# Performance work log

Measured on AMD Instinct MI355X. Metric: run time of the kernel, lower is better.

Reference implementation:

```python
import jax, jax.numpy as jnp
import numpy as np

H = 16  # n_heads


def setup_inputs() -> dict:
    key = jax.random.key(0)
    ks = jax.random.split(key, 11)
    B, S, D = 2, 2048, 1024
    def rn(k, shape, scale=1.0):
        return jax.random.normal(k, shape, dtype=jnp.float32) * scale
    w_scale = 1.0 / np.sqrt(D)
    return {
        "queries": rn(ks[0], (B, S, D)),
        "keys": rn(ks[1], (B, S, D)),
        "values": rn(ks[2], (B, S, D)),
        "Wq": rn(ks[3], (D, D), w_scale), "bq": rn(ks[4], (D,), 0.02),
        "Wk": rn(ks[5], (D, D), w_scale), "bk": rn(ks[6], (D,), 0.02),
        "Wv": rn(ks[7], (D, D), w_scale), "bv": rn(ks[8], (D,), 0.02),
        "Wo": rn(ks[9], (D, D), w_scale), "bo": rn(ks[10], (D,), 0.02),
    }


def _split_heads(x, h):
    # [B, S, D] -> [B, h, S, D/h]
    B, S, D = x.shape
    return x.reshape(B, S, h, D // h).transpose(0, 2, 1, 3)


def reference(queries, keys, values, Wq, bq, Wk, bk, Wv, bv, Wo, bo):
    B, S, D = queries.shape
    Q = _split_heads(queries @ Wq + bq, H)  # [B,h,S,dk]
    K = _split_heads(keys @ Wk + bk, H)
    V = _split_heads(values @ Wv + bv, H)
    # Faithful quirk: scale by sqrt(seq_len), not sqrt(d_k)
    factor = jnp.sqrt(jnp.asarray(S, dtype=Q.dtype))
    scores = jnp.einsum("bhqd,bhkd->bhqk", Q, K) / factor  # [B,h,S,S]
    weights = jax.nn.softmax(scores, axis=-1)
    attn = jnp.einsum("bhqk,bhkd->bhqd", weights, V)  # [B,h,S,dk]
    attn = attn.transpose(0, 2, 1, 3).reshape(B, S, D)  # [B,S,D]
    return attn @ Wo + bo
```

## Files before the change

### kernel.cpp

```cpp
#include <hip/hip_runtime.h>

typedef unsigned short ushort_t;
typedef unsigned int uint_t;
typedef __attribute__((ext_vector_type(8))) short short8;
typedef __attribute__((ext_vector_type(4))) float floatx4;

#define QSCALE 0.03187936f

__device__ __forceinline__ ushort_t f2bf(float f) {
    union { float f; uint_t u; } c; c.f = f;
    uint_t u = c.u;
    return (ushort_t)((u + 0x7fffu + ((u >> 16) & 1u)) >> 16);
}
__device__ __forceinline__ floatx4 mfma16x32(short8 a, short8 b, floatx4 c) {
    return __builtin_amdgcn_mfma_f32_16x16x32_bf16(a, b, c, 0, 0, 0);
}
__device__ __forceinline__ floatx4 zero4() { floatx4 z = {0.f, 0.f, 0.f, 0.f}; return z; }

__device__ __forceinline__ void gload16(const ushort_t* g, ushort_t* l) {
    __builtin_amdgcn_global_load_lds(
        (const __attribute__((address_space(1))) void*)g,
        (__attribute__((address_space(3))) void*)l, 16, 0, 0);
}

__global__ __launch_bounds__(256) void cvt_bf16(
    const float* __restrict__ src, ushort_t* __restrict__ dst)
{
    const int i = (blockIdx.x * 256 + threadIdx.x) * 8;
    float4 f0 = *(const float4*)(src + i);
    float4 f1 = *(const float4*)(src + i + 4);
    __align__(16) ushort_t t[8];
    t[0] = f2bf(f0.x); t[1] = f2bf(f0.y); t[2] = f2bf(f0.z); t[3] = f2bf(f0.w);
    t[4] = f2bf(f1.x); t[5] = f2bf(f1.y); t[6] = f2bf(f1.z); t[7] = f2bf(f1.w);
    *(uint4*)(dst + i) = *(uint4*)t;
}

__global__ __launch_bounds__(256) void transpose_w(
    const float* __restrict__ W0, const float* __restrict__ W1,
    const float* __restrict__ W2, const float* __restrict__ W3,
    ushort_t* __restrict__ WT)
{
    __shared__ ushort_t tile[64][65];
    const float* W = (blockIdx.y == 0) ? W0 : (blockIdx.y == 1) ? W1
                   : (blockIdx.y == 2) ? W2 : W3;
    ushort_t* dst = WT + (size_t)blockIdx.y * (1024 * 1024);
    const int t = threadIdx.x;
    const int r = t >> 2, p = t & 3;
    const int j0 = (blockIdx.x & 15) << 6, k0 = (blockIdx.x >> 4) << 6;

    const float* src = W + (size_t)(k0 + r) * 1024 + j0 + p * 16;
    float4 f0 = *(const float4*)(src);
    float4 f1 = *(const float4*)(src + 4);
    float4 f2 = *(const float4*)(src + 8);
    float4 f3 = *(const float4*)(src + 12);
    ushort_t* tr = &tile[r][p * 16];
    tr[0] = f2bf(f0.x); tr[1] = f2bf(f0.y); tr[2]  = f2bf(f0.z); tr[3]  = f2bf(f0.w);
    tr[4] = f2bf(f1.x); tr[5] = f2bf(f1.y); tr[6]  = f2bf(f1.z); tr[7]  = f2bf(f1.w);
    tr[8] = f2bf(f2.x); tr[9] = f2bf(f2.y); tr[10] = f2bf(f2.z); tr[11] = f2bf(f2.w);
    tr[12] = f2bf(f3.x); tr[13] = f2bf(f3.y); tr[14] = f2bf(f3.z); tr[15] = f2bf(f3.w);
    __syncthreads();
    __align__(16) ushort_t buf[16];
#pragma unroll
    for (int i = 0; i < 16; ++i) buf[i] = tile[p * 16 + i][r];
    ushort_t* o = dst + (size_t)(j0 + r) * 1024 + k0 + p * 16;
    *(uint4*)(o)     = *(uint4*)(buf);
    *(uint4*)(o + 8) = *(uint4*)(buf + 8);
}

__global__ __launch_bounds__(256) void gemm_bt(
    const ushort_t* __restrict__ A0, const ushort_t* __restrict__ A1,
    const ushort_t* __restrict__ A2, const ushort_t* __restrict__ A3,
    const ushort_t* __restrict__ WT,
    const float* __restrict__ b0, const float* __restrict__ b1,
    const float* __restrict__ b2, const float* __restrict__ b3,
    ushort_t* __restrict__ Dq, ushort_t* __restrict__ Dk,
    ushort_t* __restrict__ Dv, float* __restrict__ Dout, int zbase)
{
    __shared__ __align__(16) ushort_t As[128 * 32];
    __shared__ __align__(16) ushort_t Bs[128 * 32];

    const int mode = blockIdx.z + zbase;
    const ushort_t* A = (mode == 0) ? A0 : (mode == 1) ? A1 : (mode == 2) ? A2 : A3;
    const float* bias = (mode == 0) ? b0 : (mode == 1) ? b1 : (mode == 2) ? b2 : b3;
    const ushort_t* Bt = WT + (size_t)mode * 1048576;

    const int tid = threadIdx.x;
    const int lane = tid & 63, wid = tid >> 6;
    const int quad = lane >> 4, l16 = lane & 15;
    const int wm = wid >> 1, wn = wid & 1;
    const int row0 = blockIdx.y << 7, col0 = blockIdx.x << 7;

    floatx4 acc[4][4];
#pragma unroll
    for (int i = 0; i < 4; ++i)
#pragma unroll
        for (int j = 0; j < 4; ++j) acc[i][j] = zero4();

    const int i0 = tid, i1 = 256 + tid;
    const int r0_ = i0 >> 2, c0_ = (i0 & 3) ^ (r0_ & 3);
    const int r1_ = i1 >> 2, c1_ = (i1 & 3) ^ (r1_ & 3);
    const ushort_t* gA0 = A  + (size_t)(row0 + r0_) * 1024 + c0_ * 8;
    const ushort_t* gA1 = A  + (size_t)(row0 + r1_) * 1024 + c1_ * 8;
    const ushort_t* gB0 = Bt + (size_t)(col0 + r0_) * 1024 + c0_ * 8;
    const ushort_t* gB1 = Bt + (size_t)(col0 + r1_) * 1024 + c1_ * 8;
    ushort_t* lA0 = As + i0 * 8;  ushort_t* lA1 = As + i1 * 8;
    ushort_t* lB0 = Bs + i0 * 8;  ushort_t* lB1 = Bs + i1 * 8;

    const int ra = wm * 64 + l16, rb = wn * 64 + l16;
    const int sa_off = (quad ^ (l16 & 3)) * 8;

    for (int k0 = 0; k0 < 1024; k0 += 32) {
        __syncthreads();
        gload16(gA0 + k0, lA0);
        gload16(gA1 + k0, lA1);
        gload16(gB0 + k0, lB0);
        gload16(gB1 + k0, lB1);
        __syncthreads();

        short8 af[4], bf[4];
#pragma unroll
        for (int i = 0; i < 4; ++i)
            af[i] = *(const short8*)(As + (ra + i * 16) * 32 + sa_off);
#pragma unroll
        for (int j = 0; j < 4; ++j)
            bf[j] = *(const short8*)(Bs + (rb + j * 16) * 32 + sa_off);
#pragma unroll
        for (int i = 0; i < 4; ++i)
#pragma unroll
            for (int j = 0; j < 4; ++j)
                acc[i][j] = mfma16x32(af[i], bf[j], acc[i][j]);
    }

    const float sc = (mode == 0) ? QSCALE : 1.f;
#pragma unroll
    for (int i = 0; i < 4; ++i) {
#pragma unroll
        for (int j = 0; j < 4; ++j) {
            const int c = col0 + wn * 64 + j * 16 + l16;
            const float bv = bias[c];
#pragma unroll
            for (int rr = 0; rr < 4; ++rr) {
                const int r = row0 + wm * 64 + i * 16 + quad * 4 + rr;
                const float v = (acc[i][j][rr] + bv) * sc;
                if (mode <= 1) {
                    const int b = r >> 11, s = r & 2047, h = c >> 6, d = c & 63;
                    ushort_t* D = (mode == 0) ? Dq : Dk;
                    D[(((b * 16 + h) * 2048 + s) << 6) + d] = f2bf(v);
                } else if (mode == 2) {
                    const int b = r >> 11, s = r & 2047, h = c >> 6, d = c & 63;
                    Dv[(((b * 16 + h) * 64 + d) << 11) + s] = f2bf(v);
                } else {
                    Dout[(size_t)r * 1024 + c] = v;
                }
            }
        }
    }
}

__global__ __launch_bounds__(256) void attn64(
    const ushort_t* __restrict__ Q, const ushort_t* __restrict__ K,
    const ushort_t* __restrict__ Vt, ushort_t* __restrict__ Out)
{
    __shared__ __align__(16) ushort_t Ks[64 * 64];
    __shared__ __align__(16) ushort_t Vs[64 * 64];

    const int tid = threadIdx.x;
    const int lane = tid & 63, wid = tid >> 6;
    const int quad = lane >> 4, l16 = lane & 15;
    const int bh = blockIdx.y;
    const int q0 = blockIdx.x << 6;

    const ushort_t* Qh = Q + (size_t)bh * (2048 * 64);
    const ushort_t* Kh = K + (size_t)bh * (2048 * 64);
    const ushort_t* Vh = Vt + (size_t)bh * (64 * 2048);

    const int qr = q0 + wid * 16 + l16;
    const short8 qf0 = *(const short8*)(Qh + (size_t)qr * 64 + quad * 8);
    const short8 qf1 = *(const short8*)(Qh + (size_t)qr * 64 + 32 + quad * 8);

    float l_st = 0.f;
    floatx4 o_acc[4];
#pragma unroll
    for (int d = 0; d < 4; ++d) o_acc[d] = zero4();

    const int i0 = tid, i1 = 256 + tid;
    const int kr0 = i0 >> 3, kc0 = (i0 & 7) ^ (kr0 & 7);
    const int kr1 = i1 >> 3, kc1 = (i1 & 7) ^ (kr1 & 7);
    const ushort_t* gK0 = Kh + (size_t)kr0 * 64 + kc0 * 8;
    const ushort_t* gK1 = Kh + (size_t)kr1 * 64 + kc1 * 8;
    const ushort_t* gV0 = Vh + (size_t)kr0 * 2048 + kc0 * 8;
    const ushort_t* gV1 = Vh + (size_t)kr1 * 2048 + kc1 * 8;
    ushort_t* lK0 = Ks + i0 * 8;  ushort_t* lK1 = Ks + i1 * 8;
    ushort_t* lV0 = Vs + i0 * 8;  ushort_t* lV1 = Vs + i1 * 8;

    const int l7 = l16 & 7;

    for (int kt = 0; kt < 2048; kt += 64) {
        __syncthreads();
        gload16(gK0 + (size_t)kt * 64, lK0);
        gload16(gK1 + (size_t)kt * 64, lK1);
        gload16(gV0 + kt, lV0);
        gload16(gV1 + kt, lV1);
        __syncthreads();

        floatx4 sa[4];
#pragma unroll
        for (int g = 0; g < 4; ++g) {
            const int row = g * 16 + l16;
            const short8 kf0 = *(const short8*)(Ks + row * 64 + ((quad ^ l7) * 8));
            const short8 kf1 = *(const short8*)(Ks + row * 64 + (((quad + 4) ^ l7) * 8));
            sa[g] = mfma16x32(kf0, qf0, zero4());
            sa[g] = mfma16x32(kf1, qf1, sa[g]);
        }

#pragma unroll
        for (int g = 0; g < 4; ++g) {
            uint_t ub[4];
#pragma unroll
            for (int r = 0; r < 4; ++r) {
                const float e = __builtin_amdgcn_exp2f(fminf(sa[g][r], 80.f));
                const uint_t u = __float_as_uint(e) & 0xffff0000u;
                l_st += __uint_as_float(u);
                ub[r] = u;
            }
            union { uint_t u[4]; short8 s; } pc;
            pc.u[0] = (ub[0] >> 16) | ub[1];
            pc.u[1] = (ub[2] >> 16) | ub[3];
            pc.u[2] = 0u; pc.u[3] = 0u;
            const short8 pf = pc.s;

#pragma unroll
            for (int db = 0; db < 4; ++db) {
                const int vrow = db * 16 + l16;
                const int ch = g * 2 + (quad >> 1);
                const ushort_t* vp =
                    Vs + vrow * 64 + ((ch ^ (l16 & 7)) * 8) + (quad & 1) * 4;
                union { uint_t u[4]; short8 s; } vc;
                vc.u[0] = *(const uint_t*)(vp);
                vc.u[1] = *(const uint_t*)(vp + 2);
                vc.u[2] = 0u; vc.u[3] = 0u;
                o_acc[db] = mfma16x32(pf, vc.s, o_acc[db]);
            }
        }
    }

    l_st += __shfl_xor(l_st, 16);
    l_st += __shfl_xor(l_st, 32);

    const int b = bh >> 4, h = bh & 15;
    const int s0 = q0 + wid * 16 + quad * 4;
#pragma unroll
    for (int r = 0; r < 4; ++r) {
        const float lr = __shfl(l_st, quad * 4 + r);
        const float inv = 1.f / lr;
#pragma unroll
        for (int db = 0; db < 4; ++db) {
            const float v = o_acc[db][r] * inv;
            Out[(size_t)(b * 2048 + s0 + r) * 1024 + h * 64 + db * 16 + l16] = f2bf(v);
        }
    }
}

extern "C" void kernel_launch(void* const* d_in, const int* in_sizes, int n_in,
                              void* d_out, int out_size, void* d_ws, size_t ws_size,
                              hipStream_t stream) {
    const float* queries = (const float*)d_in[0];
    const float* keys    = (const float*)d_in[1];
    const float* values  = (const float*)d_in[2];
    const float* Wq = (const float*)d_in[3];
    const float* bq = (const float*)d_in[4];
    const float* Wk = (const float*)d_in[5];
    const float* bk = (const float*)d_in[6];
    const float* Wv = (const float*)d_in[7];
    const float* bv = (const float*)d_in[8];
    const float* Wo = (const float*)d_in[9];
    const float* bo = (const float*)d_in[10];
    float* out = (float*)d_out;

    char* ws = (char*)d_ws;
    const size_t MB = 1024 * 1024;
    ushort_t* WT = (ushort_t*)(ws);
    dim3 tb(256);

    transpose_w<<<dim3(256, 4), tb, 0, stream>>>(Wq, Wk, Wv, Wo, WT);

    if (ws_size >= 64 * MB) {
        ushort_t* Qb  = (ushort_t*)(ws + 8 * MB);
        ushort_t* Kb  = (ushort_t*)(ws + 16 * MB);
        ushort_t* Vb  = (ushort_t*)(ws + 24 * MB);
        ushort_t* Qp  = (ushort_t*)(ws + 32 * MB);
        ushort_t* Kp  = (ushort_t*)(ws + 40 * MB);
        ushort_t* Vtp = (ushort_t*)(ws + 48 * MB);
        ushort_t* An  = (ushort_t*)(ws + 56 * MB);
        cvt_bf16<<<dim3(2048), tb, 0, stream>>>(queries, Qb);
        cvt_bf16<<<dim3(2048), tb, 0, stream>>>(keys, Kb);
        cvt_bf16<<<dim3(2048), tb, 0, stream>>>(values, Vb);
        gemm_bt<<<dim3(8, 32, 3), tb, 0, stream>>>(Qb, Kb, Vb, An, WT,
            bq, bk, bv, bo, Qp, Kp, Vtp, out, 0);
        attn64<<<dim3(32, 32), tb, 0, stream>>>(Qp, Kp, Vtp, An);
        gemm_bt<<<dim3(8, 32, 1), tb, 0, stream>>>(Qb, Kb, Vb, An, WT,
            bq, bk, bv, bo, Qp, Kp, Vtp, out, 3);
    } else {
        ushort_t* Xb  = (ushort_t*)(ws + 8 * MB);
        ushort_t* An  = (ushort_t*)(ws + 8 * MB);
        ushort_t* Qp  = (ushort_t*)(ws + 16 * MB);
        ushort_t* Kp  = (ushort_t*)(ws + 24 * MB);
        ushort_t* Vtp = (ushort_t*)(ws + 32 * MB);
        cvt_bf16<<<dim3(2048), tb, 0, stream>>>(queries, Xb);
        gemm_bt<<<dim3(8, 32, 1), tb, 0, stream>>>(Xb, Xb, Xb, An, WT,
            bq, bk, bv, bo, Qp, Kp, Vtp, out, 0);
        cvt_bf16<<<dim3(2048), tb, 0, stream>>>(keys, Xb);
        gemm_bt<<<dim3(8, 32, 1), tb, 0, stream>>>(Xb, Xb, Xb, An, WT,
            bq, bk, bv, bo, Qp, Kp, Vtp, out, 1);
        cvt_bf16<<<dim3(2048), tb, 0, stream>>>(values, Xb);
        gemm_bt<<<dim3(8, 32, 1), tb, 0, stream>>>(Xb, Xb, Xb, An, WT,
            bq, bk, bv, bo, Qp, Kp, Vtp, out, 2);
        attn64<<<dim3(32, 32), tb, 0, stream>>>(Qp, Kp, Vtp, An);
        gemm_bt<<<dim3(8, 32, 1), tb, 0, stream>>>(Xb, Xb, Xb, An, WT,
            bq, bk, bv, bo, Qp, Kp, Vtp, out, 3);
    }
}
```

Baseline: 263.4 us.

## Use full K=32 MFMA in PV, merge conversions, add 64-row output GEMM

The attention PV step now packs two 16-key groups into one 16x16x32 bf16 MFMA instead of zero-padding half of each operand, which halves the PV MFMA count. The three fp32-to-bf16 conversion launches are merged into one kernel. The output projection moves to a dedicated 64x128-tile GEMM so it launches more blocks across the CUs. attn64 also gets a launch_bounds occupancy hint, and the low-workspace path is restructured.

```diff
diff --git a/kernel.cpp b/kernel.cpp
--- a/kernel.cpp
+++ b/kernel.cpp
@@ -24,9 +24,15 @@
 }
 
 __global__ __launch_bounds__(256) void cvt_bf16(
-    const float* __restrict__ src, ushort_t* __restrict__ dst)
-{
-    const int i = (blockIdx.x * 256 + threadIdx.x) * 8;
+    const float* __restrict__ s0, const float* __restrict__ s1,
+    const float* __restrict__ s2, ushort_t* __restrict__ d0,
+    ushort_t* __restrict__ d1, ushort_t* __restrict__ d2)
+{
+    const int which = blockIdx.x >> 11;
+    const int blk = blockIdx.x & 2047;
+    const float* src = (which == 0) ? s0 : (which == 1) ? s1 : s2;
+    ushort_t* dst = (which == 0) ? d0 : (which == 1) ? d1 : d2;
+    const int i = (blk * 256 + threadIdx.x) * 8;
     float4 f0 = *(const float4*)(src + i);
     float4 f1 = *(const float4*)(src + i + 4);
     __align__(16) ushort_t t[8];
@@ -69,19 +75,18 @@
 
 __global__ __launch_bounds__(256) void gemm_bt(
     const ushort_t* __restrict__ A0, const ushort_t* __restrict__ A1,
-    const ushort_t* __restrict__ A2, const ushort_t* __restrict__ A3,
-    const ushort_t* __restrict__ WT,
+    const ushort_t* __restrict__ A2, const ushort_t* __restrict__ WT,
     const float* __restrict__ b0, const float* __restrict__ b1,
-    const float* __restrict__ b2, const float* __restrict__ b3,
+    const float* __restrict__ b2,
     ushort_t* __restrict__ Dq, ushort_t* __restrict__ Dk,
-    ushort_t* __restrict__ Dv, float* __restrict__ Dout, int zbase)
+    ushort_t* __restrict__ Dv, int zbase)
 {
     __shared__ __align__(16) ushort_t As[128 * 32];
     __shared__ __align__(16) ushort_t Bs[128 * 32];
 
     const int mode = blockIdx.z + zbase;
-    const ushort_t* A = (mode == 0) ? A0 : (mode == 1) ? A1 : (mode == 2) ? A2 : A3;
-    const float* bias = (mode == 0) ? b0 : (mode == 1) ? b1 : (mode == 2) ? b2 : b3;
+    const ushort_t* A = (mode == 0) ? A0 : (mode == 1) ? A1 : A2;
+    const float* bias = (mode == 0) ? b0 : (mode == 1) ? b1 : b2;
     const ushort_t* Bt = WT + (size_t)mode * 1048576;
 
     const int tid = threadIdx.x;
@@ -142,22 +147,84 @@
             for (int rr = 0; rr < 4; ++rr) {
                 const int r = row0 + wm * 64 + i * 16 + quad * 4 + rr;
                 const float v = (acc[i][j][rr] + bv) * sc;
+                const int b = r >> 11, s = r & 2047, h = c >> 6, d = c & 63;
                 if (mode <= 1) {
-                    const int b = r >> 11, s = r & 2047, h = c >> 6, d = c & 63;
                     ushort_t* D = (mode == 0) ? Dq : Dk;
                     D[(((b * 16 + h) * 2048 + s) << 6) + d] = f2bf(v);
-                } else if (mode == 2) {
-                    const int b = r >> 11, s = r & 2047, h = c >> 6, d = c & 63;
+                } else {
                     Dv[(((b * 16 + h) * 64 + d) << 11) + s] = f2bf(v);
-                } else {
-                    Dout[(size_t)r * 1024 + c] = v;
                 }
             }
         }
     }
 }
 
-__global__ __launch_bounds__(256) void attn64(
+__global__ __launch_bounds__(256) void gemm64(
+    const ushort_t* __restrict__ A, const ushort_t* __restrict__ Bt,
+    const float* __restrict__ bias, float* __restrict__ Dout)
+{
+    __shared__ __align__(16) ushort_t As[64 * 32];
+    __shared__ __align__(16) ushort_t Bs[128 * 32];
+    const int tid = threadIdx.x;
+    const int lane = tid & 63, wid = tid >> 6;
+    const int quad = lane >> 4, l16 = lane & 15;
+    const int wm = wid >> 1, wn = wid & 1;
+    const int row0 = blockIdx.y << 6, col0 = blockIdx.x << 7;
+
+    floatx4 acc[2][4];
+#pragma unroll
+    for (int i = 0; i < 2; ++i)
+#pragma unroll
+        for (int j = 0; j < 4; ++j) acc[i][j] = zero4();
+
+    const int rA = tid >> 2, cA = (tid & 3) ^ (rA & 3);
+    const ushort_t* gA = A + (size_t)(row0 + rA) * 1024 + cA * 8;
+    ushort_t* lA = As + tid * 8;
+    const int i0 = tid, i1 = 256 + tid;
+    const int rB0 = i0 >> 2, cB0 = (i0 & 3) ^ (rB0 & 3);
+    const int rB1 = i1 >> 2, cB1 = (i1 & 3) ^ (rB1 & 3);
+    const ushort_t* gB0 = Bt + (size_t)(col0 + rB0) * 1024 + cB0 * 8;
+    const ushort_t* gB1 = Bt + (size_t)(col0 + rB1) * 1024 + cB1 * 8;
+    ushort_t* lB0 = Bs + i0 * 8;  ushort_t* lB1 = Bs + i1 * 8;
+
+    const int sa_off = (quad ^ (l16 & 3)) * 8;
+
+    for (int k0 = 0; k0 < 1024; k0 += 32) {
+        __syncthreads();
+        gload16(gA + k0, lA);
+        gload16(gB0 + k0, lB0);
+        gload16(gB1 + k0, lB1);
+        __syncthreads();
+
+        short8 af[2], bf[4];
+#pragma unroll
+        for (int i = 0; i < 2; ++i)
+            af[i] = *(const short8*)(As + (wm * 32 + i * 16 + l16) * 32 + sa_off);
+#pragma unroll
+        for (int j = 0; j < 4; ++j)
+            bf[j] = *(const short8*)(Bs + (wn * 64 + j * 16 + l16) * 32 + sa_off);
+#pragma unroll
+        for (int i = 0; i < 2; ++i)
+#pragma unroll
+            for (int j = 0; j < 4; ++j)
+                acc[i][j] = mfma16x32(af[i], bf[j], acc[i][j]);
+    }
+
+#pragma unroll
+    for (int i = 0; i < 2; ++i)
+#pragma unroll
+        for (int j = 0; j < 4; ++j) {
+            const int c = col0 + wn * 64 + j * 16 + l16;
+            const float bv = bias[c];
+#pragma unroll
+            for (int rr = 0; rr < 4; ++rr) {
+                const int r = row0 + wm * 32 + i * 16 + quad * 4 + rr;
+                Dout[(size_t)r * 1024 + c] = acc[i][j][rr] + bv;
+            }
+        }
+}
+
+__global__ __launch_bounds__(256, 4) void attn64(
     const ushort_t* __restrict__ Q, const ushort_t* __restrict__ K,
     const ushort_t* __restrict__ Vt, ushort_t* __restrict__ Out)
 {
@@ -194,6 +261,7 @@
     ushort_t* lV0 = Vs + i0 * 8;  ushort_t* lV1 = Vs + i1 * 8;
 
     const int l7 = l16 & 7;
+    const int q2 = quad >> 1, q1 = (quad & 1) * 4;
 
     for (int kt = 0; kt < 2048; kt += 64) {
         __syncthreads();
@@ -214,31 +282,32 @@
         }
 
 #pragma unroll
-        for (int g = 0; g < 4; ++g) {
-            uint_t ub[4];
-#pragma unroll
-            for (int r = 0; r < 4; ++r) {
+        for (int G = 0; G < 2; ++G) {
+            uint_t ub[8];
+#pragma unroll
+            for (int t = 0; t < 8; ++t) {
+                const int g = G * 2 + (t >> 2), r = t & 3;
                 const float e = __builtin_amdgcn_exp2f(fminf(sa[g][r], 80.f));
                 const uint_t u = __float_as_uint(e) & 0xffff0000u;
                 l_st += __uint_as_float(u);
-                ub[r] = u;
+                ub[t] = u;
             }
             union { uint_t u[4]; short8 s; } pc;
             pc.u[0] = (ub[0] >> 16) | ub[1];
             pc.u[1] = (ub[2] >> 16) | ub[3];
-            pc.u[2] = 0u; pc.u[3] = 0u;
+            pc.u[2] = (ub[4] >> 16) | ub[5];
+            pc.u[3] = (ub[6] >> 16) | ub[7];
             const short8 pf = pc.s;
 
+            const int ch0 = ((4 * G + q2) ^ l7) * 8;
+            const int ch1 = ((4 * G + 2 + q2) ^ l7) * 8;
 #pragma unroll
             for (int db = 0; db < 4; ++db) {
-                const int vrow = db * 16 + l16;
-                const int ch = g * 2 + (quad >> 1);
-                const ushort_t* vp =
-                    Vs + vrow * 64 + ((ch ^ (l16 & 7)) * 8) + (quad & 1) * 4;
+                const int vbase = (db * 16 + l16) * 64 + q1;
+                const uint2 v0 = *(const uint2*)(Vs + vbase + ch0);
+                const uint2 v1 = *(const uint2*)(Vs + vbase + ch1);
                 union { uint_t u[4]; short8 s; } vc;
-                vc.u[0] = *(const uint_t*)(vp);
-                vc.u[1] = *(const uint_t*)(vp + 2);
-                vc.u[2] = 0u; vc.u[3] = 0u;
+                vc.u[0] = v0.x; vc.u[1] = v0.y; vc.u[2] = v1.x; vc.u[3] = v1.y;
                 o_acc[db] = mfma16x32(pf, vc.s, o_acc[db]);
             }
         }
@@ -280,6 +349,7 @@
     char* ws = (char*)d_ws;
     const size_t MB = 1024 * 1024;
     ushort_t* WT = (ushort_t*)(ws);
+    const ushort_t* WoT = WT + 3 * 1048576;
     dim3 tb(256);
 
     transpose_w<<<dim3(256, 4), tb, 0, stream>>>(Wq, Wk, Wv, Wo, WT);
@@ -292,31 +362,23 @@
         ushort_t* Kp  = (ushort_t*)(ws + 40 * MB);
         ushort_t* Vtp = (ushort_t*)(ws + 48 * MB);
         ushort_t* An  = (ushort_t*)(ws + 56 * MB);
-        cvt_bf16<<<dim3(2048), tb, 0, stream>>>(queries, Qb);
-        cvt_bf16<<<dim3(2048), tb, 0, stream>>>(keys, Kb);
-        cvt_bf16<<<dim3(2048), tb, 0, stream>>>(values, Vb);
-        gemm_bt<<<dim3(8, 32, 3), tb, 0, stream>>>(Qb, Kb, Vb, An, WT,
-            bq, bk, bv, bo, Qp, Kp, Vtp, out, 0);
+        cvt_bf16<<<dim3(6144), tb, 0, stream>>>(queries, keys, values, Qb, Kb, Vb);
+        gemm_bt<<<dim3(8, 32, 3), tb, 0, stream>>>(Qb, Kb, Vb, WT,
+            bq, bk, bv, Qp, Kp, Vtp, 0);
         attn64<<<dim3(32, 32), tb, 0, stream>>>(Qp, Kp, Vtp, An);
-        gemm_bt<<<dim3(8, 32, 1), tb, 0, stream>>>(Qb, Kb, Vb, An, WT,
-            bq, bk, bv, bo, Qp, Kp, Vtp, out, 3);
+        gemm64<<<dim3(8, 64), tb, 0, stream>>>(An, WoT, bo, out);
     } else {
-        ushort_t* Xb  = (ushort_t*)(ws + 8 * MB);
-        ushort_t* An  = (ushort_t*)(ws + 8 * MB);
-        ushort_t* Qp  = (ushort_t*)(ws + 16 * MB);
-        ushort_t* Kp  = (ushort_t*)(ws + 24 * MB);
-        ushort_t* Vtp = (ushort_t*)(ws + 32 * MB);
-        cvt_bf16<<<dim3(2048), tb, 0, stream>>>(queries, Xb);
-        gemm_bt<<<dim3(8, 32, 1), tb, 0, stream>>>(Xb, Xb, Xb, An, WT,
-            bq, bk, bv, bo, Qp, Kp, Vtp, out, 0);
-        cvt_bf16<<<dim3(2048), tb, 0, stream>>>(keys, Xb);
-        gemm_bt<<<dim3(8, 32, 1), tb, 0, stream>>>(Xb, Xb, Xb, An, WT,
-            bq, bk, bv, bo, Qp, Kp, Vtp, out, 1);
-        cvt_bf16<<<dim3(2048), tb, 0, stream>>>(values, Xb);
-        gemm_bt<<<dim3(8, 32, 1), tb, 0, stream>>>(Xb, Xb, Xb, An, WT,
-            bq, bk, bv, bo, Qp, Kp, Vtp, out, 2);
-        attn64<<<dim3(32, 32), tb, 0, stream>>>(Qp, Kp, Vtp, An);
-        gemm_bt<<<dim3(8, 32, 1), tb, 0, stream>>>(Xb, Xb, Xb, An, WT,
-            bq, bk, bv, bo, Qp, Kp, Vtp, out, 3);
-    }
-}
+        ushort_t* buf1 = (ushort_t*)(ws + 8 * MB);
+        ushort_t* buf2 = (ushort_t*)(ws + 16 * MB);
+        ushort_t* Qp   = (ushort_t*)(ws + 24 * MB);
+        ushort_t* Kp   = (ushort_t*)(ws + 32 * MB);
+        cvt_bf16<<<dim3(4096), tb, 0, stream>>>(queries, keys, keys, buf1, buf2, buf2);
+        gemm_bt<<<dim3(8, 32, 2), tb, 0, stream>>>(buf1, buf2, buf2, WT,
+            bq, bk, bk, Qp, Kp, Kp, 0);
+        cvt_bf16<<<dim3(2048), tb, 0, stream>>>(values, values, values, buf1, buf1, buf1);
+        gemm_bt<<<dim3(8, 32, 1), tb, 0, stream>>>(buf1, buf1, buf1, WT,
+            bv, bv, bv, buf2, buf2, buf2, 2);
+        attn64<<<dim3(32, 32), tb, 0, stream>>>(Qp, Kp, buf2, buf1);
+        gemm64<<<dim3(8, 64), tb, 0, stream>>>(buf1, WoT, bo, out);
+    }
+}
```

Result: faster. 237.3 us (-9.9%).
